# Optimization experiments

Measured on AMD Instinct MI355X. Metric: run time of the kernel, lower is better.

## Reference

```python
import jax, jax.numpy as jnp
import numpy as np
import math

N_HEAD = 16
STRIDE = 128
C = 8


def _sparse_causal_mask(q_len, k_len):
    # Mirrors LingLongAttention._sparse_causal_mask (static, host-side numpy).
    cols = np.arange(k_len)
    rows = np.arange(k_len)[:, None]
    strided = (cols % STRIDE) >= (STRIDE - C)          # last C cols of each stride block
    local = (cols[None, :] // STRIDE) == (rows // STRIDE)  # same stride block as query
    causal = cols[None, :] <= rows
    layout = (strided[None, :] | local) & causal       # [k_len, k_len]
    return jnp.asarray(layout[k_len - q_len:])         # [q_len, k_len]


def setup_inputs() -> dict:
    key = jax.random.key(0)
    k1, k2, k3 = jax.random.split(key, 3)
    B, S, E = 2, 2048, 1024
    return {
        "hidden_states": jax.random.normal(k1, (B, S, E), dtype=jnp.float32),
        "W_attn": jax.random.normal(k2, (E, 3 * E), dtype=jnp.float32) * 0.02,
        "b_attn": jnp.zeros((3 * E,), dtype=jnp.float32),
        "W_proj": jax.random.normal(k3, (E, E), dtype=jnp.float32) * 0.02,
        "b_proj": jnp.zeros((E,), dtype=jnp.float32),
    }


def reference(hidden_states, W_attn, b_attn, W_proj, b_proj):
    B, S, E = hidden_states.shape
    H = N_HEAD
    D = E // H
    # Conv1D: x @ W + b, then split into q,k,v
    qkv = hidden_states @ W_attn + b_attn                 # [B,S,3E]
    q, k, v = jnp.split(qkv, 3, axis=-1)
    split = lambda t: t.reshape(B, S, H, D).transpose(0, 2, 1, 3)  # [B,H,S,D]
    q, k, v = split(q), split(k), split(v)
    scale = jnp.asarray(1.0 / math.sqrt(D), dtype=q.dtype)
    scores = jnp.einsum("bhqd,bhkd->bhqk", q, k) * scale  # [B,H,S,S]
    mask = _sparse_causal_mask(S, S)[None, None]          # [1,1,S,S]
    mask_value = jnp.asarray(jnp.finfo(scores.dtype).min, dtype=scores.dtype)
    scores = jnp.where(mask, scores, mask_value)
    attn = jax.nn.softmax(scores, axis=-1)
    out = jnp.einsum("bhqk,bhkd->bhqd", attn, v)          # [B,H,S,D]
    out = out.transpose(0, 2, 1, 3).reshape(B, S, E)      # merge heads
    return out @ W_proj + b_proj
```

## Files before the change

### kernel.cpp

```cpp
#include <hip/hip_runtime.h>
#include <hip/hip_bf16.h>
#include <stdint.h>

typedef unsigned short u16;
typedef uint32_t u32;
typedef short s16x8 __attribute__((ext_vector_type(8)));
typedef float f32x4 __attribute__((ext_vector_type(4)));

#define SDIM 2048
#define EDIM 1024

static __device__ __forceinline__ float b2f(u16 v) {
    union { float f; u32 u; } c; c.u = ((u32)v) << 16; return c.f;
}
static __device__ __forceinline__ u16 f2b(float f) {
    union { float f; u32 u; } c; c.f = f;
    u32 u = c.u;
    u32 r = (u + 0x7FFFu + ((u >> 16) & 1u)) >> 16;
    return (u16)r;
}
static __device__ __forceinline__ void gll16(const u16* g, u16* l) {
    __builtin_amdgcn_global_load_lds(
        (const __attribute__((address_space(1))) void*)g,
        (__attribute__((address_space(3))) void*)l, 16, 0, 0);
}

__global__ void k_detect(const u16* __restrict__ x, int* __restrict__ flag) {
    __shared__ int cnt;
    if (threadIdx.x == 0) cnt = 0;
    __syncthreads();
    u16 v = x[threadIdx.x * 2];
    int e = (v >> 7) & 0xFF;
    int ok = (e >= 90 && e <= 144) ? 1 : 0;
    atomicAdd(&cnt, ok);
    __syncthreads();
    if (threadIdx.x == 0) flag[0] = (cnt >= 192) ? 1 : 0;
}

__global__ void k_convx(const void* __restrict__ X, u16* __restrict__ Xb,
                        const int* __restrict__ flag) {
    if (flag[0]) return;
    long i = ((long)blockIdx.x * 256 + threadIdx.x) * 8;
    const float* s = (const float*)X;
    u16 o[8];
    for (int j = 0; j < 8; ++j) o[j] = f2b(s[i + j]);
    *(uint4*)&Xb[i] = *(uint4*)o;
}

__global__ __launch_bounds__(256) void k_trans(
    const void* __restrict__ Wa, const void* __restrict__ Wp,
    u16* __restrict__ WtA, u16* __restrict__ WtP, const int* __restrict__ flag) {
    int z = blockIdx.z;
    if (z == 1 && blockIdx.x >= 16) return;
    const void* src = z ? Wp : Wa;
    u16* dst = z ? WtP : WtA;
    int Nsrc = z ? 1024 : 3072;
    int n0 = blockIdx.x * 64, k0 = blockIdx.y * 64;
    int t = threadIdx.x, f = flag[0];
    __shared__ u16 L[64 * 72];
    int r = t >> 2, c0 = (t & 3) * 16;
    u16 val[16];
    if (f) {
        const u16* s = (const u16*)src + (size_t)(k0 + r) * Nsrc + n0 + c0;
        *(uint4*)&val[0] = *(const uint4*)s;
        *(uint4*)&val[8] = *(const uint4*)(s + 8);
    } else {
        const float* s = (const float*)src + (size_t)(k0 + r) * Nsrc + n0 + c0;
        for (int j = 0; j < 16; ++j) val[j] = f2b(s[j]);
    }
    for (int j = 0; j < 16; ++j) L[(c0 + j) * 72 + r] = val[j];
    __syncthreads();
    int kc0 = (t & 3) * 16;
    uint4 o0 = *(const uint4*)&L[r * 72 + kc0];
    uint4 o1 = *(const uint4*)&L[r * 72 + kc0 + 8];
    u16* d = dst + (size_t)(n0 + r) * 1024 + k0 + kc0;
    *(uint4*)d = o0;
    *(uint4*)(d + 8) = o1;
}

__global__ __launch_bounds__(256) void k_gemm1(
    const u16* __restrict__ Xraw, const u16* __restrict__ Xb,
    const u16* __restrict__ Bt, const void* __restrict__ bias,
    u16* __restrict__ C, const int* __restrict__ flag) {
    const int K = 1024, N = 3072;
    __shared__ u16 As[128 * 64];
    __shared__ u16 Bs[128 * 64];
    int f = flag[0];
    const u16* A = f ? Xraw : Xb;
    int t = threadIdx.x, wave = t >> 6, lane = t & 63;
    int m0 = blockIdx.y * 128, n0 = blockIdx.x * 128;
    int wm = (wave >> 1) * 64, wn = (wave & 1) * 64;
    int lm = lane & 15, lk = (lane >> 4) * 8;
    int sr = t >> 2, sc = (t & 3) * 8;
    const u16* Ap = A + (size_t)(m0 + sr) * K + sc;
    const u16* Bp = Bt + (size_t)(n0 + sr) * K + sc;
    u16* Asw = As + wave * 512;
    u16* Bsw = Bs + wave * 512;

    f32x4 acc[4][4];
    f32x4 z = {0.f, 0.f, 0.f, 0.f};
    for (int mi = 0; mi < 4; ++mi)
        for (int ni = 0; ni < 4; ++ni) acc[mi][ni] = z;

    for (int k0 = 0; k0 < K; k0 += 64) {
        gll16(Ap + k0, Asw);
        gll16(Ap + (size_t)64 * K + k0, Asw + 2048);
        gll16(Ap + k0 + 32, Asw + 4096);
        gll16(Ap + (size_t)64 * K + k0 + 32, Asw + 6144);
        gll16(Bp + k0, Bsw);
        gll16(Bp + (size_t)64 * K + k0, Bsw + 2048);
        gll16(Bp + k0 + 32, Bsw + 4096);
        gll16(Bp + (size_t)64 * K + k0 + 32, Bsw + 6144);
        __syncthreads();
        for (int kh = 0; kh < 2; ++kh) {
            const u16* Ab = As + kh * 4096;
            const u16* Bb = Bs + kh * 4096;
            s16x8 af[4], bfr[4];
            for (int mi = 0; mi < 4; ++mi)
                af[mi] = *(const s16x8*)&Ab[(wm + mi * 16 + lm) * 32 + lk];
            for (int ni = 0; ni < 4; ++ni)
                bfr[ni] = *(const s16x8*)&Bb[(wn + ni * 16 + lm) * 32 + lk];
            for (int mi = 0; mi < 4; ++mi)
                for (int ni = 0; ni < 4; ++ni)
                    acc[mi][ni] = __builtin_amdgcn_mfma_f32_16x16x32_bf16(
                        af[mi], bfr[ni], acc[mi][ni], 0, 0, 0);
        }
        __syncthreads();
    }

    int cn = lane & 15, cr = (lane >> 4) * 4;
    for (int ni = 0; ni < 4; ++ni) {
        int gn = n0 + wn + ni * 16 + cn;
        float bb = f ? b2f(((const u16*)bias)[gn]) : ((const float*)bias)[gn];
        for (int mi = 0; mi < 4; ++mi)
            for (int r = 0; r < 4; ++r) {
                int gm = m0 + wm + mi * 16 + cr + r;
                C[(size_t)gm * N + gn] = f2b(acc[mi][ni][r] + bb);
            }
    }
}

__global__ __launch_bounds__(256) void k_gemm2(
    const u16* __restrict__ A, const u16* __restrict__ Bt, const void* __restrict__ bias,
    u16* __restrict__ Cb, float* __restrict__ Cf, const int* __restrict__ flag) {
    const int K = 1024, N = 1024;
    __shared__ u16 As[64 * 32];
    __shared__ u16 Bs[128 * 32];
    int t = threadIdx.x, wave = t >> 6, lane = t & 63;
    int m0 = blockIdx.y * 64, n0 = blockIdx.x * 128;
    int wm = (wave >> 1) * 32, wn = (wave & 1) * 64;
    int lm = lane & 15, lk = (lane >> 4) * 8;
    int sr = t >> 2, sc = (t & 3) * 8;
    const u16* Ap = A + (size_t)(m0 + sr) * K + sc;
    const u16* Bp = Bt + (size_t)(n0 + sr) * K + sc;
    u16* Asw = As + wave * 512;
    u16* Bsw = Bs + wave * 512;

    f32x4 acc[2][4];
    f32x4 z = {0.f, 0.f, 0.f, 0.f};
    for (int mi = 0; mi < 2; ++mi)
        for (int ni = 0; ni < 4; ++ni) acc[mi][ni] = z;

    for (int k0 = 0; k0 < K; k0 += 32) {
        gll16(Ap + k0, Asw);
        gll16(Bp + k0, Bsw);
        gll16(Bp + (size_t)64 * K + k0, Bsw + 2048);
        __syncthreads();
        s16x8 af[2], bfr[4];
        for (int mi = 0; mi < 2; ++mi)
            af[mi] = *(const s16x8*)&As[(wm + mi * 16 + lm) * 32 + lk];
        for (int ni = 0; ni < 4; ++ni)
            bfr[ni] = *(const s16x8*)&Bs[(wn + ni * 16 + lm) * 32 + lk];
        for (int mi = 0; mi < 2; ++mi)
            for (int ni = 0; ni < 4; ++ni)
                acc[mi][ni] = __builtin_amdgcn_mfma_f32_16x16x32_bf16(
                    af[mi], bfr[ni], acc[mi][ni], 0, 0, 0);
        __syncthreads();
    }

    int f = flag[0];
    int store_f32 = (f == 0);
    int cn = lane & 15, cr = (lane >> 4) * 4;
    for (int ni = 0; ni < 4; ++ni) {
        int gn = n0 + wn + ni * 16 + cn;
        float bb = f ? b2f(((const u16*)bias)[gn]) : ((const float*)bias)[gn];
        for (int mi = 0; mi < 2; ++mi)
            for (int r = 0; r < 4; ++r) {
                int gm = m0 + wm + mi * 16 + cr + r;
                float v = acc[mi][ni][r] + bb;
                size_t o = (size_t)gm * N + gn;
                if (store_f32) Cf[o] = v;
                else           Cb[o] = f2b(v);
            }
    }
}

#define VP 264
#define PP 264
__global__ __launch_bounds__(256) void k_attn3(const u16* __restrict__ QKV,
                                               u16* __restrict__ AO) {
    int bx = blockIdx.x, h = blockIdx.y, b = blockIdx.z;
    int qb = bx >> 1, sb = bx & 1;
    int t = threadIdx.x, lane = t & 63, wave = t >> 6;
    int lm = lane & 15, q4 = lane >> 4;
    int nstr = qb << 3;
    int nk = nstr + (sb << 6) + 64;
    int r0 = (qb << 7) + (sb << 6);

    __shared__ char smem[79872];
    u16* Vts = (u16*)smem;
    u16* Qs  = (u16*)(smem + 33792);
    u16* Ks  = (u16*)(smem + 33792 + 9216);
    u16* Ps  = (u16*)(smem + 33792);

    const u16* base = QKV + (size_t)b * SDIM * 3072;

    for (int c = t; c < 512; c += 256) {
        int r = c >> 3, d0 = (c & 7) << 3;
        *(uint4*)&Qs[r * 72 + d0] =
            *(const uint4*)(base + (size_t)(r0 + r) * 3072 + h * 64 + d0);
    }
    uint4 zz = {0u, 0u, 0u, 0u};
    for (int c = t; c < 2048; c += 256) {
        int i = c >> 3, d0 = (c & 7) << 3;
        uint4 kv = zz;
        if (i < nk) {
            int key = (i < nstr) ? (((i >> 3) << 7) + 120 + (i & 7))
                                 : ((qb << 7) + (i - nstr));
            kv = *(const uint4*)(base + (size_t)key * 3072 + 1024 + h * 64 + d0);
        }
        *(uint4*)&Ks[i * 72 + d0] = kv;
    }
    {
        int i0 = (t & 31) * 8, d0 = (t >> 5) * 8;
        u16 m8[8][8];
        for (int r = 0; r < 8; ++r) {
            int i = i0 + r;
            uint4 vv = zz;
            if (i < nk) {
                int key = (i < nstr) ? (((i >> 3) << 7) + 120 + (i & 7))
                                     : ((qb << 7) + (i - nstr));
                vv = *(const uint4*)(base + (size_t)key * 3072 + 2048 + h * 64 + d0);
            }
            *(uint4*)m8[r] = vv;
        }
        for (int j = 0; j < 8; ++j) {
            u16 o[8];
            for (int r = 0; r < 8; ++r) o[r] = m8[r][j];
            *(uint4*)&Vts[(d0 + j) * VP + i0] = *(uint4*)o;
        }
    }
    __syncthreads();

    f32x4 acc[16];
    f32x4 z4 = {0.f, 0.f, 0.f, 0.f};
    for (int ni = 0; ni < 16; ++ni) acc[ni] = z4;
    s16x8 af0 = *(const s16x8*)&Qs[(wave * 16 + lm) * 72 + q4 * 8];
    s16x8 af1 = *(const s16x8*)&Qs[(wave * 16 + lm) * 72 + 32 + q4 * 8];
    for (int ni = 0; ni < 16; ++ni) {
        s16x8 bf0 = *(const s16x8*)&Ks[(ni * 16 + lm) * 72 + q4 * 8];
        s16x8 bf1 = *(const s16x8*)&Ks[(ni * 16 + lm) * 72 + 32 + q4 * 8];
        acc[ni] = __builtin_amdgcn_mfma_f32_16x16x32_bf16(af0, bf0, acc[ni], 0, 0, 0);
        acc[ni] = __builtin_amdgcn_mfma_f32_16x16x32_bf16(af1, bf1, acc[ni], 0, 0, 0);
    }
    __syncthreads();

    float mx[4] = {-3e38f, -3e38f, -3e38f, -3e38f};
    for (int ni = 0; ni < 16; ++ni) {
        int i = ni * 16 + lm;
        for (int reg = 0; reg < 4; ++reg) {
            int rl = (sb << 6) + wave * 16 + q4 * 4 + reg;
            bool valid = (i < nstr) || ((i - nstr) <= rl);
            float v = valid ? acc[ni][reg] * 0.125f : -3e38f;
            acc[ni][reg] = v;
            mx[reg] = fmaxf(mx[reg], v);
        }
    }
    for (int reg = 0; reg < 4; ++reg)
        for (int off = 1; off < 16; off <<= 1)
            mx[reg] = fmaxf(mx[reg], __shfl_xor(mx[reg], off, 64));
    float sm[4] = {0.f, 0.f, 0.f, 0.f};
    for (int ni = 0; ni < 16; ++ni)
        for (int reg = 0; reg < 4; ++reg) {
            float e = __expf(acc[ni][reg] - mx[reg]);
            acc[ni][reg] = e;
            sm[reg] += e;
        }
    for (int reg = 0; reg < 4; ++reg)
        for (int off = 1; off < 16; off <<= 1)
            sm[reg] += __shfl_xor(sm[reg], off, 64);
    float inv[4];
    for (int reg = 0; reg < 4; ++reg) inv[reg] = 1.f / sm[reg];

    for (int ni = 0; ni < 16; ++ni) {
        int i = ni * 16 + lm;
        for (int reg = 0; reg < 4; ++reg)
            Ps[(wave * 16 + q4 * 4 + reg) * PP + i] = f2b(acc[ni][reg]);
    }
    __syncthreads();

    f32x4 acc2[4];
    for (int ni2 = 0; ni2 < 4; ++ni2) acc2[ni2] = z4;
    for (int k0 = 0; k0 < 256; k0 += 32) {
        s16x8 pf = *(const s16x8*)&Ps[(wave * 16 + lm) * PP + k0 + q4 * 8];
        for (int ni2 = 0; ni2 < 4; ++ni2) {
            s16x8 vf = *(const s16x8*)&Vts[(ni2 * 16 + lm) * VP + k0 + q4 * 8];
            acc2[ni2] = __builtin_amdgcn_mfma_f32_16x16x32_bf16(pf, vf, acc2[ni2], 0, 0, 0);
        }
    }
    int srow = r0 + wave * 16 + q4 * 4;
    for (int ni2 = 0; ni2 < 4; ++ni2)
        for (int reg = 0; reg < 4; ++reg) {
            size_t o = ((size_t)(b * SDIM + srow + reg)) * EDIM + h * 64 + ni2 * 16 + lm;
            AO[o] = f2b(acc2[ni2][reg] * inv[reg]);
        }
}

extern "C" void kernel_launch(void* const* d_in, const int* in_sizes, int n_in,
                              void* d_out, int out_size, void* d_ws, size_t ws_size,
                              hipStream_t stream) {
    const void* X  = d_in[0];
    const void* Wa = d_in[1];
    const void* ba = d_in[2];
    const void* Wp = d_in[3];
    const void* bp = d_in[4];

    char* w = (char*)d_ws;
    int* flag = (int*)w;
    u16* Xb   = (u16*)(w + 256);
    u16* WtA  = (u16*)(w + 8388864);
    u16* WtP  = (u16*)(w + 14688512);
    u16* QKV  = (u16*)(w + 16789760);
    u16* AO   = (u16*)(w + 41955584);

    k_detect<<<1, 256, 0, stream>>>((const u16*)X, flag);
    k_convx<<<2048, 256, 0, stream>>>(X, Xb, flag);
    k_trans<<<dim3(48, 16, 2), 256, 0, stream>>>(Wa, Wp, WtA, WtP, flag);

    k_gemm1<<<dim3(24, 32), 256, 0, stream>>>((const u16*)X, Xb, WtA, ba, QKV, flag);
    k_attn3<<<dim3(32, 16, 2), 256, 0, stream>>>(QKV, AO);
    k_gemm2<<<dim3(8, 64), 256, 0, stream>>>(AO, WtP, bp, (u16*)d_out, (float*)d_out,
                                             flag);
}
```

Measured before the change: 176.5 us.

## Fuse detect/convert/transpose prep kernels and double gemm2 K-tile

Removes the separate dtype-detection kernel and flag buffer by having each kernel sniff the input format with a wave ballot. The X conversion and weight transposes are merged into one prep launch, cutting two kernel launches and their serialization gaps. gemm2's K step grows from 32 to 64, so it runs half as many barrier-separated iterations, at the cost of more shared memory per block. Every kernel repeats the sniff read, and the heuristic now uses 64 samples instead of 256.

```diff
diff --git a/kernel.cpp b/kernel.cpp
--- a/kernel.cpp
+++ b/kernel.cpp
@@ -25,38 +25,37 @@
         (__attribute__((address_space(3))) void*)l, 16, 0, 0);
 }
 
-__global__ void k_detect(const u16* __restrict__ x, int* __restrict__ flag) {
-    __shared__ int cnt;
-    if (threadIdx.x == 0) cnt = 0;
-    __syncthreads();
-    u16 v = x[threadIdx.x * 2];
+static __device__ __forceinline__ int sniff_bf16(const u16* __restrict__ x) {
+    u16 v = x[(threadIdx.x & 63) * 2];
     int e = (v >> 7) & 0xFF;
-    int ok = (e >= 90 && e <= 144) ? 1 : 0;
-    atomicAdd(&cnt, ok);
-    __syncthreads();
-    if (threadIdx.x == 0) flag[0] = (cnt >= 192) ? 1 : 0;
-}
-
-__global__ void k_convx(const void* __restrict__ X, u16* __restrict__ Xb,
-                        const int* __restrict__ flag) {
-    if (flag[0]) return;
-    long i = ((long)blockIdx.x * 256 + threadIdx.x) * 8;
-    const float* s = (const float*)X;
-    u16 o[8];
-    for (int j = 0; j < 8; ++j) o[j] = f2b(s[i + j]);
-    *(uint4*)&Xb[i] = *(uint4*)o;
-}
-
-__global__ __launch_bounds__(256) void k_trans(
-    const void* __restrict__ Wa, const void* __restrict__ Wp,
-    u16* __restrict__ WtA, u16* __restrict__ WtP, const int* __restrict__ flag) {
+    unsigned long long m = __ballot(e >= 90 && e <= 144);
+    return __popcll(m) >= 48;
+}
+
+__global__ __launch_bounds__(256) void k_prep(
+    const void* __restrict__ X, const void* __restrict__ Wa,
+    const void* __restrict__ Wp, u16* __restrict__ Xb,
+    u16* __restrict__ WtA, u16* __restrict__ WtP) {
+    int f = sniff_bf16((const u16*)X);
     int z = blockIdx.z;
+    int t = threadIdx.x;
+    if (z == 2) {
+        if (f) return;
+        const float* s = (const float*)X;
+        int bid = blockIdx.y * 48 + blockIdx.x;
+        for (int c = bid; c < 2048; c += 768) {
+            long i = ((long)c * 256 + t) * 8;
+            u16 o[8];
+            for (int j = 0; j < 8; ++j) o[j] = f2b(s[i + j]);
+            *(uint4*)&Xb[i] = *(uint4*)o;
+        }
+        return;
+    }
     if (z == 1 && blockIdx.x >= 16) return;
     const void* src = z ? Wp : Wa;
     u16* dst = z ? WtP : WtA;
     int Nsrc = z ? 1024 : 3072;
     int n0 = blockIdx.x * 64, k0 = blockIdx.y * 64;
-    int t = threadIdx.x, f = flag[0];
     __shared__ u16 L[64 * 72];
     int r = t >> 2, c0 = (t & 3) * 16;
     u16 val[16];
@@ -70,10 +69,9 @@
     }
     for (int j = 0; j < 16; ++j) L[(c0 + j) * 72 + r] = val[j];
     __syncthreads();
-    int kc0 = (t & 3) * 16;
-    uint4 o0 = *(const uint4*)&L[r * 72 + kc0];
-    uint4 o1 = *(const uint4*)&L[r * 72 + kc0 + 8];
-    u16* d = dst + (size_t)(n0 + r) * 1024 + k0 + kc0;
+    uint4 o0 = *(const uint4*)&L[r * 72 + c0];
+    uint4 o1 = *(const uint4*)&L[r * 72 + c0 + 8];
+    u16* d = dst + (size_t)(n0 + r) * 1024 + k0 + c0;
     *(uint4*)d = o0;
     *(uint4*)(d + 8) = o1;
 }
@@ -81,11 +79,11 @@
 __global__ __launch_bounds__(256) void k_gemm1(
     const u16* __restrict__ Xraw, const u16* __restrict__ Xb,
     const u16* __restrict__ Bt, const void* __restrict__ bias,
-    u16* __restrict__ C, const int* __restrict__ flag) {
+    u16* __restrict__ C) {
     const int K = 1024, N = 3072;
     __shared__ u16 As[128 * 64];
     __shared__ u16 Bs[128 * 64];
-    int f = flag[0];
+    int f = sniff_bf16(Xraw);
     const u16* A = f ? Xraw : Xb;
     int t = threadIdx.x, wave = t >> 6, lane = t & 63;
     int m0 = blockIdx.y * 128, n0 = blockIdx.x * 128;
@@ -141,11 +139,13 @@
 }
 
 __global__ __launch_bounds__(256) void k_gemm2(
-    const u16* __restrict__ A, const u16* __restrict__ Bt, const void* __restrict__ bias,
-    u16* __restrict__ Cb, float* __restrict__ Cf, const int* __restrict__ flag) {
+    const u16* __restrict__ Xraw, const u16* __restrict__ A,
+    const u16* __restrict__ Bt, const void* __restrict__ bias,
+    u16* __restrict__ Cb, float* __restrict__ Cf) {
     const int K = 1024, N = 1024;
-    __shared__ u16 As[64 * 32];
-    __shared__ u16 Bs[128 * 32];
+    __shared__ u16 As[64 * 64];
+    __shared__ u16 Bs[128 * 64];
+    int f = sniff_bf16(Xraw);
     int t = threadIdx.x, wave = t >> 6, lane = t & 63;
     int m0 = blockIdx.y * 64, n0 = blockIdx.x * 128;
     int wm = (wave >> 1) * 32, wn = (wave & 1) * 64;
@@ -161,24 +161,30 @@
     for (int mi = 0; mi < 2; ++mi)
         for (int ni = 0; ni < 4; ++ni) acc[mi][ni] = z;
 
-    for (int k0 = 0; k0 < K; k0 += 32) {
+    for (int k0 = 0; k0 < K; k0 += 64) {
         gll16(Ap + k0, Asw);
+        gll16(Ap + k0 + 32, Asw + 2048);
         gll16(Bp + k0, Bsw);
         gll16(Bp + (size_t)64 * K + k0, Bsw + 2048);
+        gll16(Bp + k0 + 32, Bsw + 4096);
+        gll16(Bp + (size_t)64 * K + k0 + 32, Bsw + 6144);
         __syncthreads();
-        s16x8 af[2], bfr[4];
-        for (int mi = 0; mi < 2; ++mi)
-            af[mi] = *(const s16x8*)&As[(wm + mi * 16 + lm) * 32 + lk];
-        for (int ni = 0; ni < 4; ++ni)
-            bfr[ni] = *(const s16x8*)&Bs[(wn + ni * 16 + lm) * 32 + lk];
-        for (int mi = 0; mi < 2; ++mi)
+        for (int kh = 0; kh < 2; ++kh) {
+            const u16* Ab = As + kh * 2048;
+            const u16* Bb = Bs + kh * 4096;
+            s16x8 af[2], bfr[4];
+            for (int mi = 0; mi < 2; ++mi)
+                af[mi] = *(const s16x8*)&Ab[(wm + mi * 16 + lm) * 32 + lk];
             for (int ni = 0; ni < 4; ++ni)
-                acc[mi][ni] = __builtin_amdgcn_mfma_f32_16x16x32_bf16(
-                    af[mi], bfr[ni], acc[mi][ni], 0, 0, 0);
+                bfr[ni] = *(const s16x8*)&Bb[(wn + ni * 16 + lm) * 32 + lk];
+            for (int mi = 0; mi < 2; ++mi)
+                for (int ni = 0; ni < 4; ++ni)
+                    acc[mi][ni] = __builtin_amdgcn_mfma_f32_16x16x32_bf16(
+                        af[mi], bfr[ni], acc[mi][ni], 0, 0, 0);
+        }
         __syncthreads();
     }
 
-    int f = flag[0];
     int store_f32 = (f == 0);
     int cn = lane & 15, cr = (lane >> 4) * 4;
     for (int ni = 0; ni < 4; ++ni) {
@@ -326,19 +332,15 @@
     const void* bp = d_in[4];
 
     char* w = (char*)d_ws;
-    int* flag = (int*)w;
-    u16* Xb   = (u16*)(w + 256);
-    u16* WtA  = (u16*)(w + 8388864);
-    u16* WtP  = (u16*)(w + 14688512);
-    u16* QKV  = (u16*)(w + 16789760);
-    u16* AO   = (u16*)(w + 41955584);
-
-    k_detect<<<1, 256, 0, stream>>>((const u16*)X, flag);
-    k_convx<<<2048, 256, 0, stream>>>(X, Xb, flag);
-    k_trans<<<dim3(48, 16, 2), 256, 0, stream>>>(Wa, Wp, WtA, WtP, flag);
-
-    k_gemm1<<<dim3(24, 32), 256, 0, stream>>>((const u16*)X, Xb, WtA, ba, QKV, flag);
+    u16* Xb   = (u16*)(w);
+    u16* WtA  = (u16*)(w + 8388608);
+    u16* WtP  = (u16*)(w + 14680064);
+    u16* QKV  = (u16*)(w + 16777216);
+    u16* AO   = (u16*)(w + 41943040);
+
+    k_prep<<<dim3(48, 16, 3), 256, 0, stream>>>(X, Wa, Wp, Xb, WtA, WtP);
+    k_gemm1<<<dim3(24, 32), 256, 0, stream>>>((const u16*)X, Xb, WtA, ba, QKV);
     k_attn3<<<dim3(32, 16, 2), 256, 0, stream>>>(QKV, AO);
-    k_gemm2<<<dim3(8, 64), 256, 0, stream>>>(AO, WtP, bp, (u16*)d_out, (float*)d_out,
-                                             flag);
-}
+    k_gemm2<<<dim3(8, 64), 256, 0, stream>>>((const u16*)X, AO, WtP, bp,
+                                             (u16*)d_out, (float*)d_out);
+}
```

New measurement: 169.6 us. -3.9%, faster.
